# Kernel tuning notes

Measured on AMD Instinct MI355X. Metric: run time of the kernel, lower is better.

Reference implementation:

```python
import jax, jax.numpy as jnp
import numpy as np
import math

B, N, NODE_DIM, EDGE_DIM, HID, NH = 2, 384, 128, 128, 128, 8
HD = HID // NH  # head_dim = 16


def _layernorm(x, g, b, eps=1e-5):
    m = jnp.mean(x, axis=-1, keepdims=True)
    v = jnp.var(x, axis=-1, keepdims=True)
    return (x - m) * jax.lax.rsqrt(v + eps) * g + b


def setup_inputs() -> dict:
    key = jax.random.key(0)
    ks = jax.random.split(key, 16)
    w = lambda k, s: jax.random.normal(k, s, jnp.float32) * 0.05
    return {
        "node_features": jax.random.normal(ks[0], (B, N, NODE_DIM), jnp.float32),
        "edge_features": jax.random.normal(ks[1], (B, N, N, EDGE_DIM), jnp.float32),
        "adj_mask": jax.random.randint(ks[2], (B, N, N), 0, 2, jnp.int32),
        "W_node": w(ks[3], (NODE_DIM, HID)), "b_node": jnp.zeros((HID,), jnp.float32),
        "W_q": w(ks[4], (HID, HID)), "b_q": jnp.zeros((HID,), jnp.float32),
        "W_k": w(ks[5], (HID, HID)), "b_k": jnp.zeros((HID,), jnp.float32),
        "W_v": w(ks[6], (HID, HID)), "b_v": jnp.zeros((HID,), jnp.float32),
        "W_edge": w(ks[7], (EDGE_DIM, HID)), "b_edge": jnp.zeros((HID,), jnp.float32),
        "W_gate": w(ks[8], (EDGE_DIM, HID)), "b_gate": jnp.zeros((HID,), jnp.float32),
        "W_out": w(ks[9], (HID, HID)), "b_out": jnp.zeros((HID,), jnp.float32),
        "W_eout": w(ks[10], (HID, EDGE_DIM)), "b_eout": jnp.zeros((EDGE_DIM,), jnp.float32),
        "g1": jnp.ones((HID,), jnp.float32), "be1": jnp.zeros((HID,), jnp.float32),
        "g2": jnp.ones((EDGE_DIM,), jnp.float32), "be2": jnp.zeros((EDGE_DIM,), jnp.float32),
    }


def reference(node_features, edge_features, adj_mask,
              W_node, b_node, W_q, b_q, W_k, b_k, W_v, b_v,
              W_edge, b_edge, W_gate, b_gate, W_out, b_out,
              W_eout, b_eout, g1, be1, g2, be2):
    b, n, _ = node_features.shape
    h = node_features @ W_node + b_node          # (B,N,HID)
    residual = h
    Q = (h @ W_q + b_q).reshape(b, n, NH, HD)
    K = (h @ W_k + b_k).reshape(b, n, NH, HD)
    V = (h @ W_v + b_v).reshape(b, n, NH, HD)
    scores = jnp.einsum('bihd,bjhd->bhij', Q, K) / math.sqrt(HD)  # (B,NH,N,N)
    # edge-gated bias
    edge_h = (edge_features @ W_edge + b_edge).reshape(b, n, n, NH, HD)
    edge_gate = jax.nn.sigmoid(edge_features @ W_gate + b_gate).reshape(b, n, n, NH, HD)
    edge_attn = jnp.sum(edge_h * edge_gate, axis=-1)  # (B,N,N,NH)
    scores = scores + jnp.transpose(edge_attn, (0, 3, 1, 2))
    # adjacency mask
    scores = jnp.where(adj_mask[:, None, :, :] == 0, jnp.float32(-1e9), scores)
    attn = jax.nn.softmax(scores, axis=-1)  # dropout = identity (eval)
    attn_out = jnp.einsum('bhij,bjhd->bihd', attn, V).reshape(b, n, HID)
    h = _layernorm(residual + (attn_out @ W_out + b_out), g1, be1)
    # edge update: mean attention over heads gates (src+tgt)/2
    attn_mean = jnp.mean(attn, axis=1)  # (B,N,N)
    pair = 0.5 * (h[:, :, None, :] + h[:, None, :, :])  # (B,N,N,HID)
    edge_update = attn_mean[..., None] * pair
    edge_out = _layernorm(edge_features + (edge_update @ W_eout + b_eout), g2, be2)
    return h, edge_out
```

## Files before the change

### kernel.cpp

```cpp
#include <hip/hip_runtime.h>
#include <hip/hip_bf16.h>

#define NN 384
#define HIDDIM 128
#define NHEADS 8
#define HD 16
#define LOCAL_E (NN*NN)
#define NE (2*LOCAL_E)
#define NNODE (2*NN)

typedef __attribute__((ext_vector_type(8))) __bf16 bf16x8;
typedef __attribute__((ext_vector_type(4))) float f32x4;

__global__ void prep_w(const float* __restrict__ W_edge, const float* __restrict__ W_gate,
                       bf16x8* __restrict__ Wg) {
    int gid = blockIdx.x * blockDim.x + threadIdx.x;
    int n16  = gid & 15;
    int quad = (gid >> 4) & 3;
    int kkl  = (gid >> 6) & 1;
    int np   = (gid >> 7) & 15;
    int kkh  = (gid >> 11) & 1;
    int n = np * 16 + n16;
    int k0 = (kkh * 2 + kkl) * 32 + quad * 8;
    const float* src = (n < 128) ? (W_edge + n) : (W_gate + (n - 128));
    bf16x8 v;
#pragma unroll
    for (int j = 0; j < 8; ++j) v[j] = (__bf16)src[(size_t)(k0 + j) * 128];
    Wg[gid] = v;
}

__global__ __launch_bounds__(128) void k1_proj(
    const float* __restrict__ nf,
    const float* __restrict__ Wn, const float* __restrict__ bn,
    const float* __restrict__ Wq, const float* __restrict__ bq,
    const float* __restrict__ Wk, const float* __restrict__ bk,
    const float* __restrict__ Wv, const float* __restrict__ bv,
    float* __restrict__ h_res, float* __restrict__ Q,
    float* __restrict__ K, float* __restrict__ V)
{
    __shared__ float xf[8][128];
    __shared__ float hf[8][128];
    int t = threadIdx.x;
    int r0 = blockIdx.x * 8;
    for (int r = 0; r < 8; ++r) xf[r][t] = nf[(size_t)(r0 + r) * 128 + t];
    __syncthreads();
    float acc[8];
#pragma unroll
    for (int r = 0; r < 8; ++r) acc[r] = bn[t];
    for (int k = 0; k < 128; ++k) {
        float w = Wn[k * 128 + t];
#pragma unroll
        for (int r = 0; r < 8; ++r) acc[r] += xf[r][k] * w;
    }
    for (int r = 0; r < 8; ++r) { h_res[(size_t)(r0 + r) * 128 + t] = acc[r]; hf[r][t] = acc[r]; }
    __syncthreads();
    const float* Ws[3] = {Wq, Wk, Wv};
    const float* bs[3] = {bq, bk, bv};
    float* Os[3] = {Q, K, V};
#pragma unroll
    for (int m = 0; m < 3; ++m) {
        float a2[8];
#pragma unroll
        for (int r = 0; r < 8; ++r) a2[r] = bs[m][t];
        for (int k = 0; k < 128; ++k) {
            float w = Ws[m][k * 128 + t];
#pragma unroll
            for (int r = 0; r < 8; ++r) a2[r] += hf[r][k] * w;
        }
        int hh = t >> 4, d = t & 15;
        for (int r = 0; r < 8; ++r) {
            int g = r0 + r;
            int b = g / NN, i = g - b * NN;
            Os[m][(size_t)((b * NHEADS + hh) * NN + i) * HD + d] = a2[r];
        }
    }
}

__global__ __launch_bounds__(512, 4) void k2_edge(
    const float* __restrict__ EF, const bf16x8* __restrict__ Wg,
    const float* __restrict__ b_edge, const float* __restrict__ b_gate,
    float* __restrict__ edge_attn)
{
    __shared__ bf16x8 Ash[1024];
    __shared__ bf16x8 Bsh[2048];
    int t = threadIdx.x;
    int lane = t & 63;
    int w = t >> 6;
    int wm = w & 1, wn = w >> 1;
    int e_base = blockIdx.x * 128;

    f32x4 acc[4][4];
    f32x4 zero = {0.f, 0.f, 0.f, 0.f};
#pragma unroll
    for (int i = 0; i < 4; ++i)
#pragma unroll
        for (int j = 0; j < 4; ++j) acc[i][j] = zero;

    for (int kkh = 0; kkh < 2; ++kkh) {
#pragma unroll
        for (int p = 0; p < 4; ++p) {
            int g = p * 512 + t;
            Bsh[g] = Wg[kkh * 2048 + g];
        }
#pragma unroll
        for (int p = 0; p < 2; ++p) {
            int gid = p * 512 + t;
            int m16 = gid & 15, quad = (gid >> 4) & 3, kkl = (gid >> 6) & 1, ip = gid >> 7;
            int row = ip * 16 + m16;
            const float4* src4 = (const float4*)(EF + (size_t)(e_base + row) * 128
                                                 + (kkh * 2 + kkl) * 32 + quad * 8);
            float4 f0 = src4[0], f1 = src4[1];
            bf16x8 v;
            v[0] = (__bf16)f0.x; v[1] = (__bf16)f0.y; v[2] = (__bf16)f0.z; v[3] = (__bf16)f0.w;
            v[4] = (__bf16)f1.x; v[5] = (__bf16)f1.y; v[6] = (__bf16)f1.z; v[7] = (__bf16)f1.w;
            Ash[gid] = v;
        }
        __syncthreads();
#pragma unroll
        for (int kkl = 0; kkl < 2; ++kkl) {
            bf16x8 af[4], bfh[2], bfg[2];
#pragma unroll
            for (int i = 0; i < 4; ++i) {
                int ip = wm * 4 + i;
                af[i] = Ash[(ip * 2 + kkl) * 64 + lane];
            }
#pragma unroll
            for (int j = 0; j < 2; ++j) {
                int nph = wn * 2 + j;
                bfh[j] = Bsh[(nph * 2 + kkl) * 64 + lane];
                bfg[j] = Bsh[((nph + 8) * 2 + kkl) * 64 + lane];
            }
#pragma unroll
            for (int i = 0; i < 4; ++i) {
#pragma unroll
                for (int j = 0; j < 2; ++j) {
                    acc[i][j]     = __builtin_amdgcn_mfma_f32_16x16x32_bf16(af[i], bfh[j], acc[i][j], 0, 0, 0);
                    acc[i][j + 2] = __builtin_amdgcn_mfma_f32_16x16x32_bf16(af[i], bfg[j], acc[i][j + 2], 0, 0, 0);
                }
            }
        }
        __syncthreads();
    }

    int n16 = lane & 15, quad = lane >> 4;
#pragma unroll
    for (int j = 0; j < 2; ++j) {
        int c = wn * 32 + j * 16 + n16;
        float bh = b_edge[c], bg = b_gate[c];
        int head = wn * 2 + j;
#pragma unroll
        for (int i = 0; i < 4; ++i) {
#pragma unroll
            for (int r = 0; r < 4; ++r) {
                float hv = acc[i][j][r] + bh;
                float gv = acc[i][j + 2][r] + bg;
                float v = hv * (1.f / (1.f + __expf(-gv)));
                v += __shfl_xor(v, 1);
                v += __shfl_xor(v, 2);
                v += __shfl_xor(v, 4);
                v += __shfl_xor(v, 8);
                if (n16 == 0) {
                    int m = wm * 64 + i * 16 + quad * 4 + r;
                    int e = e_base + m;
                    int b = e / LOCAL_E;
                    int local = e - b * LOCAL_E;
                    edge_attn[(size_t)(b * NHEADS + head) * LOCAL_E + local] = v;
                }
            }
        }
    }
}

__global__ __launch_bounds__(128) void k3_attn(
    const float* __restrict__ Q, const float* __restrict__ K, const float* __restrict__ V,
    const float* __restrict__ edge_attn, const int* __restrict__ adj,
    float* __restrict__ am, float* __restrict__ attn_out)
{
    __shared__ float Kh[NN * 17];
    __shared__ float Vh[NN * 17];
    __shared__ float Qi[16 * HD];
    __shared__ float rowbuf[NN];
    __shared__ float red[2];
    __shared__ float red2[8][16];
    int t = threadIdx.x;
    int bh = blockIdx.x / 24;
    int chunk = blockIdx.x % 24;
    int b = bh >> 3;
    const float* Kbase = K + (size_t)bh * NN * HD;
    const float* Vbase = V + (size_t)bh * NN * HD;
    for (int p = 0; p < 48; ++p) {
        int idx = p * 128 + t;
        int jj = idx >> 4, dd = idx & 15;
        Kh[jj * 17 + dd] = Kbase[idx];
        Vh[jj * 17 + dd] = Vbase[idx];
    }
    Qi[t]       = Q[(size_t)bh * NN * HD + chunk * 16 * HD + t];
    Qi[t + 128] = Q[(size_t)bh * NN * HD + chunk * 16 * HD + t + 128];
    __syncthreads();
    int lane = t & 63, wid = t >> 6;
    const float* ea = edge_attn + (size_t)bh * LOCAL_E;
    const int* adjb = adj + (size_t)b * LOCAL_E;
    for (int rr = 0; rr < 16; ++rr) {
        int i = chunk * 16 + rr;
        float s[3];
#pragma unroll
        for (int jj = 0; jj < 3; ++jj) {
            int j = t + jj * 128;
            float a = 0.f;
#pragma unroll
            for (int d = 0; d < 16; ++d) a += Qi[rr * 16 + d] * Kh[j * 17 + d];
            a = a * 0.25f + ea[(size_t)i * NN + j];
            if (adjb[(size_t)i * NN + j] == 0) a = -1e9f;
            s[jj] = a;
        }
        float mx = fmaxf(s[0], fmaxf(s[1], s[2]));
#pragma unroll
        for (int o = 1; o < 64; o <<= 1) mx = fmaxf(mx, __shfl_xor(mx, o));
        if (lane == 0) red[wid] = mx;
        __syncthreads();
        mx = fmaxf(red[0], red[1]);
        __syncthreads();
        float e0 = __expf(s[0] - mx), e1 = __expf(s[1] - mx), e2 = __expf(s[2] - mx);
        float sm = e0 + e1 + e2;
#pragma unroll
        for (int o = 1; o < 64; o <<= 1) sm += __shfl_xor(sm, o);
        if (lane == 0) red[wid] = sm;
        __syncthreads();
        float inv = 1.f / (red[0] + red[1]);
        float p0 = e0 * inv, p1 = e1 * inv, p2 = e2 * inv;
        rowbuf[t] = p0; rowbuf[t + 128] = p1; rowbuf[t + 256] = p2;
        atomicAdd(am + (size_t)b * LOCAL_E + i * NN + t,       p0 * 0.125f);
        atomicAdd(am + (size_t)b * LOCAL_E + i * NN + t + 128, p1 * 0.125f);
        atomicAdd(am + (size_t)b * LOCAL_E + i * NN + t + 256, p2 * 0.125f);
        __syncthreads();
        int d = t & 15, g = t >> 4;
        float pa = 0.f;
        for (int j = g * 48; j < g * 48 + 48; ++j) pa += rowbuf[j] * Vh[j * 17 + d];
        red2[g][d] = pa;
        __syncthreads();
        if (t < 16) {
            float s2 = 0.f;
#pragma unroll
            for (int gg = 0; gg < 8; ++gg) s2 += red2[gg][t];
            attn_out[(size_t)(b * NN + i) * HIDDIM + (bh & 7) * HD + t] = s2;
        }
        __syncthreads();
    }
}

__global__ __launch_bounds__(128) void k5_hout(
    const float* __restrict__ attn_out, const float* __restrict__ h_res,
    const float* __restrict__ W_out, const float* __restrict__ b_out,
    const float* __restrict__ g1, const float* __restrict__ be1,
    const float* __restrict__ W_eout,
    float* __restrict__ h_out, float* __restrict__ hp)
{
    __shared__ float ao[8][128];
    __shared__ float hn[8][128];
    __shared__ float redA[2], redB[2];
    int t = threadIdx.x, r0 = blockIdx.x * 8;
    for (int r = 0; r < 8; ++r) ao[r][t] = attn_out[(size_t)(r0 + r) * 128 + t];
    __syncthreads();
    float acc[8];
#pragma unroll
    for (int r = 0; r < 8; ++r) acc[r] = b_out[t];
    for (int k = 0; k < 128; ++k) {
        float w = W_out[k * 128 + t];
#pragma unroll
        for (int r = 0; r < 8; ++r) acc[r] += ao[r][k] * w;
    }
    int lane = t & 63, wid = t >> 6;
    float gg = g1[t], bb = be1[t];
    for (int r = 0; r < 8; ++r) {
        float u = h_res[(size_t)(r0 + r) * 128 + t] + acc[r];
        float sv = u, sq = u * u;
#pragma unroll
        for (int o = 1; o < 64; o <<= 1) { sv += __shfl_xor(sv, o); sq += __shfl_xor(sq, o); }
        if (lane == 0) { redA[wid] = sv; redB[wid] = sq; }
        __syncthreads();
        float tot = redA[0] + redA[1], totq = redB[0] + redB[1];
        __syncthreads();
        float mean = tot * (1.f / 128.f);
        float var = totq * (1.f / 128.f) - mean * mean;
        float nv = (u - mean) * rsqrtf(var + 1e-5f) * gg + bb;
        h_out[(size_t)(r0 + r) * 128 + t] = nv;
        hn[r][t] = nv;
    }
    __syncthreads();
    float acc2[8];
#pragma unroll
    for (int r = 0; r < 8; ++r) acc2[r] = 0.f;
    for (int k = 0; k < 128; ++k) {
        float w = W_eout[k * 128 + t];
#pragma unroll
        for (int r = 0; r < 8; ++r) acc2[r] += hn[r][k] * w;
    }
    for (int r = 0; r < 8; ++r) hp[(size_t)(r0 + r) * 128 + t] = acc2[r];
}

__global__ __launch_bounds__(256) void k6_eout(
    const float* __restrict__ EF, const float* __restrict__ am,
    const float* __restrict__ hp, const float* __restrict__ b_eout,
    const float* __restrict__ g2, const float* __restrict__ be2,
    float* __restrict__ eout)
{
    int t = threadIdx.x;
    int slot = t >> 5, l = t & 31;
    int e = blockIdx.x * 8 + slot;
    int b = e / LOCAL_E;
    int local = e - b * LOCAL_E;
    int i = local / NN, j = local - i * NN;
    float a = am[e];
    const float4* ef4 = (const float4*)(EF + (size_t)e * 128);
    const float4* hpi = (const float4*)(hp + (size_t)(b * NN + i) * 128);
    const float4* hpj = (const float4*)(hp + (size_t)(b * NN + j) * 128);
    float4 ef = ef4[l];
    float4 pi = hpi[l], pj = hpj[l];
    float4 bo = ((const float4*)b_eout)[l];
    float4 u;
    u.x = ef.x + a * 0.5f * (pi.x + pj.x) + bo.x;
    u.y = ef.y + a * 0.5f * (pi.y + pj.y) + bo.y;
    u.z = ef.z + a * 0.5f * (pi.z + pj.z) + bo.z;
    u.w = ef.w + a * 0.5f * (pi.w + pj.w) + bo.w;
    float sv = u.x + u.y + u.z + u.w;
    float sq = u.x * u.x + u.y * u.y + u.z * u.z + u.w * u.w;
#pragma unroll
    for (int o = 1; o < 32; o <<= 1) { sv += __shfl_xor(sv, o); sq += __shfl_xor(sq, o); }
    float mean = sv * (1.f / 128.f);
    float var = sq * (1.f / 128.f) - mean * mean;
    float rs = rsqrtf(var + 1e-5f);
    float4 gg = ((const float4*)g2)[l], bb = ((const float4*)be2)[l];
    float4 o4;
    o4.x = (u.x - mean) * rs * gg.x + bb.x;
    o4.y = (u.y - mean) * rs * gg.y + bb.y;
    o4.z = (u.z - mean) * rs * gg.z + bb.z;
    o4.w = (u.w - mean) * rs * gg.w + bb.w;
    ((float4*)(eout + (size_t)e * 128))[l] = o4;
}

extern "C" void kernel_launch(void* const* d_in, const int* in_sizes, int n_in,
                              void* d_out, int out_size, void* d_ws, size_t ws_size,
                              hipStream_t stream) {
    (void)in_sizes; (void)n_in; (void)out_size; (void)ws_size;
    const float* nf     = (const float*)d_in[0];
    const float* ef     = (const float*)d_in[1];
    const int*   adj    = (const int*)d_in[2];
    const float* W_node = (const float*)d_in[3];
    const float* b_node = (const float*)d_in[4];
    const float* W_q    = (const float*)d_in[5];
    const float* b_q    = (const float*)d_in[6];
    const float* W_k    = (const float*)d_in[7];
    const float* b_k    = (const float*)d_in[8];
    const float* W_v    = (const float*)d_in[9];
    const float* b_v    = (const float*)d_in[10];
    const float* W_edge = (const float*)d_in[11];
    const float* b_edge = (const float*)d_in[12];
    const float* W_gate = (const float*)d_in[13];
    const float* b_gate = (const float*)d_in[14];
    const float* W_out  = (const float*)d_in[15];
    const float* b_out  = (const float*)d_in[16];
    const float* W_eout = (const float*)d_in[17];
    const float* b_eout = (const float*)d_in[18];
    const float* g1     = (const float*)d_in[19];
    const float* be1    = (const float*)d_in[20];
    const float* g2     = (const float*)d_in[21];
    const float* be2    = (const float*)d_in[22];

    float* ws = (float*)d_ws;
    float* h_res    = ws;
    float* Q        = ws + 98304;
    float* Kp       = ws + 196608;
    float* Vp       = ws + 294912;
    float* attn_out = ws + 393216;
    float* hp       = ws + 491520;
    float* am       = ws + 589824;
    bf16x8* Wg      = (bf16x8*)(ws + 884736);

    float* h_out = (float*)d_out;
    float* eout  = (float*)d_out + 98304;
    float* edge_attn = eout;

    prep_w<<<dim3(16), dim3(256), 0, stream>>>(W_edge, W_gate, Wg);
    k1_proj<<<dim3(96), dim3(128), 0, stream>>>(nf, W_node, b_node, W_q, b_q,
                                                W_k, b_k, W_v, b_v, h_res, Q, Kp, Vp);
    k2_edge<<<dim3(2304), dim3(512), 0, stream>>>(ef, Wg, b_edge, b_gate, edge_attn);
    hipMemsetAsync((void*)am, 0, (size_t)NE * sizeof(float), stream);
    k3_attn<<<dim3(384), dim3(128), 0, stream>>>(Q, Kp, Vp, edge_attn, adj, am, attn_out);
    k5_hout<<<dim3(96), dim3(128), 0, stream>>>(attn_out, h_res, W_out, b_out,
                                                g1, be1, W_eout, h_out, hp);
    k6_eout<<<dim3(36864), dim3(256), 0, stream>>>(ef, am, hp, b_eout, g2, be2, eout);
}
```

Before: 483.1 us.

## Persistent wave-tiled edge GEMM, fold mask into edge bias, drop atomics

The edge projection kernel becomes a persistent kernel. Each wave loops over 16-edge tiles, keeps all 256 weight columns resident in LDS and prefetches the next tile's edge features into registers. The adjacency mask is applied there, so the attention kernel no longer reads adj. The attention kernel is restructured to one row per wave with K/V stored transposed, with no block-level syncs, and it writes per-head attention probabilities. The atomic head-mean and its memset are removed: k6 now sums the 8 heads itself, at the cost of extra workspace and extra attention-map traffic.

```diff
diff --git a/kernel.cpp b/kernel.cpp
--- a/kernel.cpp
+++ b/kernel.cpp
@@ -7,7 +7,8 @@
 #define HD 16
 #define LOCAL_E (NN*NN)
 #define NE (2*LOCAL_E)
-#define NNODE (2*NN)
+#define NTILES (NE/16)
+#define NWAVES_K2 4096
 
 typedef __attribute__((ext_vector_type(8))) __bf16 bf16x8;
 typedef __attribute__((ext_vector_type(4))) float f32x4;
@@ -17,12 +18,11 @@
     int gid = blockIdx.x * blockDim.x + threadIdx.x;
     int n16  = gid & 15;
     int quad = (gid >> 4) & 3;
-    int kkl  = (gid >> 6) & 1;
-    int np   = (gid >> 7) & 15;
-    int kkh  = (gid >> 11) & 1;
-    int n = np * 16 + n16;
-    int k0 = (kkh * 2 + kkl) * 32 + quad * 8;
-    const float* src = (n < 128) ? (W_edge + n) : (W_gate + (n - 128));
+    int kk   = (gid >> 6) & 3;
+    int cg   = gid >> 8;
+    int col = cg * 16 + n16;
+    int k0 = kk * 32 + quad * 8;
+    const float* src = (col < 128) ? (W_edge + col) : (W_gate + (col - 128));
     bf16x8 v;
 #pragma unroll
     for (int j = 0; j < 8; ++j) v[j] = (__bf16)src[(size_t)(k0 + j) * 128];
@@ -76,175 +76,188 @@
     }
 }
 
-__global__ __launch_bounds__(512, 4) void k2_edge(
+__global__ __launch_bounds__(512, 2) void k2_edge(
     const float* __restrict__ EF, const bf16x8* __restrict__ Wg,
     const float* __restrict__ b_edge, const float* __restrict__ b_gate,
-    float* __restrict__ edge_attn)
+    const int* __restrict__ adj, float* __restrict__ ea)
 {
-    __shared__ bf16x8 Ash[1024];
-    __shared__ bf16x8 Bsh[2048];
+    __shared__ bf16x8 Bsh[4096];
     int t = threadIdx.x;
     int lane = t & 63;
     int w = t >> 6;
-    int wm = w & 1, wn = w >> 1;
-    int e_base = blockIdx.x * 128;
-
-    f32x4 acc[4][4];
-    f32x4 zero = {0.f, 0.f, 0.f, 0.f};
-#pragma unroll
-    for (int i = 0; i < 4; ++i)
-#pragma unroll
-        for (int j = 0; j < 4; ++j) acc[i][j] = zero;
-
-    for (int kkh = 0; kkh < 2; ++kkh) {
-#pragma unroll
-        for (int p = 0; p < 4; ++p) {
-            int g = p * 512 + t;
-            Bsh[g] = Wg[kkh * 2048 + g];
-        }
-#pragma unroll
-        for (int p = 0; p < 2; ++p) {
-            int gid = p * 512 + t;
-            int m16 = gid & 15, quad = (gid >> 4) & 3, kkl = (gid >> 6) & 1, ip = gid >> 7;
-            int row = ip * 16 + m16;
-            const float4* src4 = (const float4*)(EF + (size_t)(e_base + row) * 128
-                                                 + (kkh * 2 + kkl) * 32 + quad * 8);
-            float4 f0 = src4[0], f1 = src4[1];
+#pragma unroll
+    for (int p = 0; p < 8; ++p) {
+        int g = p * 512 + t;
+        Bsh[g] = Wg[g];
+    }
+    __syncthreads();
+
+    int n16 = lane & 15, quad = lane >> 4;
+    float bhv[8], bgv[8];
+#pragma unroll
+    for (int h = 0; h < 8; ++h) {
+        bhv[h] = b_edge[h * 16 + n16];
+        bgv[h] = b_gate[h * 16 + n16];
+    }
+
+    int gw = blockIdx.x * 8 + w;
+    int tile = gw;
+
+    float4 f[8];
+    const float* ar0 = EF + ((size_t)tile * 16 + n16) * 128 + quad * 8;
+#pragma unroll
+    for (int kk = 0; kk < 4; ++kk) {
+        f[2 * kk]     = *(const float4*)(ar0 + kk * 32);
+        f[2 * kk + 1] = *(const float4*)(ar0 + kk * 32 + 4);
+    }
+
+    while (tile < NTILES) {
+        int next = tile + NWAVES_K2;
+        bf16x8 af[4];
+#pragma unroll
+        for (int kk = 0; kk < 4; ++kk) {
+            float4 f0 = f[2 * kk], f1 = f[2 * kk + 1];
             bf16x8 v;
             v[0] = (__bf16)f0.x; v[1] = (__bf16)f0.y; v[2] = (__bf16)f0.z; v[3] = (__bf16)f0.w;
             v[4] = (__bf16)f1.x; v[5] = (__bf16)f1.y; v[6] = (__bf16)f1.z; v[7] = (__bf16)f1.w;
-            Ash[gid] = v;
-        }
-        __syncthreads();
-#pragma unroll
-        for (int kkl = 0; kkl < 2; ++kkl) {
-            bf16x8 af[4], bfh[2], bfg[2];
-#pragma unroll
-            for (int i = 0; i < 4; ++i) {
-                int ip = wm * 4 + i;
-                af[i] = Ash[(ip * 2 + kkl) * 64 + lane];
+            af[kk] = v;
+        }
+        if (next < NTILES) {
+            const float* ar = EF + ((size_t)next * 16 + n16) * 128 + quad * 8;
+#pragma unroll
+            for (int kk = 0; kk < 4; ++kk) {
+                f[2 * kk]     = *(const float4*)(ar + kk * 32);
+                f[2 * kk + 1] = *(const float4*)(ar + kk * 32 + 4);
             }
-#pragma unroll
-            for (int j = 0; j < 2; ++j) {
-                int nph = wn * 2 + j;
-                bfh[j] = Bsh[(nph * 2 + kkl) * 64 + lane];
-                bfg[j] = Bsh[((nph + 8) * 2 + kkl) * 64 + lane];
+        }
+
+        f32x4 acc[8][2];
+        f32x4 zero = {0.f, 0.f, 0.f, 0.f};
+#pragma unroll
+        for (int h = 0; h < 8; ++h) { acc[h][0] = zero; acc[h][1] = zero; }
+#pragma unroll
+        for (int kk = 0; kk < 4; ++kk) {
+#pragma unroll
+            for (int h = 0; h < 8; ++h) {
+                bf16x8 bh = Bsh[(h * 4 + kk) * 64 + lane];
+                bf16x8 bg = Bsh[((8 + h) * 4 + kk) * 64 + lane];
+                acc[h][0] = __builtin_amdgcn_mfma_f32_16x16x32_bf16(af[kk], bh, acc[h][0], 0, 0, 0);
+                acc[h][1] = __builtin_amdgcn_mfma_f32_16x16x32_bf16(af[kk], bg, acc[h][1], 0, 0, 0);
             }
-#pragma unroll
-            for (int i = 0; i < 4; ++i) {
-#pragma unroll
-                for (int j = 0; j < 2; ++j) {
-                    acc[i][j]     = __builtin_amdgcn_mfma_f32_16x16x32_bf16(af[i], bfh[j], acc[i][j], 0, 0, 0);
-                    acc[i][j + 2] = __builtin_amdgcn_mfma_f32_16x16x32_bf16(af[i], bfg[j], acc[i][j + 2], 0, 0, 0);
-                }
-            }
-        }
-        __syncthreads();
-    }
-
-    int n16 = lane & 15, quad = lane >> 4;
-#pragma unroll
-    for (int j = 0; j < 2; ++j) {
-        int c = wn * 32 + j * 16 + n16;
-        float bh = b_edge[c], bg = b_gate[c];
-        int head = wn * 2 + j;
-#pragma unroll
-        for (int i = 0; i < 4; ++i) {
+        }
+
+        size_t e0 = (size_t)tile * 16;
+        int b = (tile >= NTILES / 2) ? 1 : 0;
+        int local0 = (int)(e0 - (size_t)b * LOCAL_E);
+        const int* adjp = adj + (size_t)b * LOCAL_E + local0 + quad * 4;
+        int av0 = adjp[0], av1 = adjp[1], av2 = adjp[2], av3 = adjp[3];
+#pragma unroll
+        for (int h = 0; h < 8; ++h) {
+            float vr[4];
 #pragma unroll
             for (int r = 0; r < 4; ++r) {
-                float hv = acc[i][j][r] + bh;
-                float gv = acc[i][j + 2][r] + bg;
+                float hv = acc[h][0][r] + bhv[h];
+                float gv = acc[h][1][r] + bgv[h];
                 float v = hv * (1.f / (1.f + __expf(-gv)));
                 v += __shfl_xor(v, 1);
                 v += __shfl_xor(v, 2);
                 v += __shfl_xor(v, 4);
                 v += __shfl_xor(v, 8);
-                if (n16 == 0) {
-                    int m = wm * 64 + i * 16 + quad * 4 + r;
-                    int e = e_base + m;
-                    int b = e / LOCAL_E;
-                    int local = e - b * LOCAL_E;
-                    edge_attn[(size_t)(b * NHEADS + head) * LOCAL_E + local] = v;
-                }
+                vr[r] = v;
             }
-        }
-    }
-}
-
-__global__ __launch_bounds__(128) void k3_attn(
+            if (n16 == 0) {
+                float4 o;
+                o.x = av0 ? vr[0] : -1e9f;
+                o.y = av1 ? vr[1] : -1e9f;
+                o.z = av2 ? vr[2] : -1e9f;
+                o.w = av3 ? vr[3] : -1e9f;
+                *(float4*)(ea + ((size_t)(b * 8 + h)) * LOCAL_E + local0 + quad * 4) = o;
+            }
+        }
+        tile = next;
+    }
+}
+
+__global__ __launch_bounds__(256) void k3_attn(
     const float* __restrict__ Q, const float* __restrict__ K, const float* __restrict__ V,
-    const float* __restrict__ edge_attn, const int* __restrict__ adj,
-    float* __restrict__ am, float* __restrict__ attn_out)
+    const float* __restrict__ ea, float* __restrict__ attn,
+    float* __restrict__ attn_out)
 {
-    __shared__ float Kh[NN * 17];
-    __shared__ float Vh[NN * 17];
-    __shared__ float Qi[16 * HD];
-    __shared__ float rowbuf[NN];
-    __shared__ float red[2];
-    __shared__ float red2[8][16];
+    __shared__ float Kt[16 * 385];
+    __shared__ float Vt[16 * 385];
+    __shared__ float Qi[256];
+    __shared__ float prow[4][384];
     int t = threadIdx.x;
     int bh = blockIdx.x / 24;
     int chunk = blockIdx.x % 24;
-    int b = bh >> 3;
+    int b = bh >> 3, h = bh & 7;
     const float* Kbase = K + (size_t)bh * NN * HD;
     const float* Vbase = V + (size_t)bh * NN * HD;
-    for (int p = 0; p < 48; ++p) {
-        int idx = p * 128 + t;
-        int jj = idx >> 4, dd = idx & 15;
-        Kh[jj * 17 + dd] = Kbase[idx];
-        Vh[jj * 17 + dd] = Vbase[idx];
-    }
-    Qi[t]       = Q[(size_t)bh * NN * HD + chunk * 16 * HD + t];
-    Qi[t + 128] = Q[(size_t)bh * NN * HD + chunk * 16 * HD + t + 128];
-    __syncthreads();
-    int lane = t & 63, wid = t >> 6;
-    const float* ea = edge_attn + (size_t)bh * LOCAL_E;
-    const int* adjb = adj + (size_t)b * LOCAL_E;
-    for (int rr = 0; rr < 16; ++rr) {
-        int i = chunk * 16 + rr;
-        float s[3];
-#pragma unroll
-        for (int jj = 0; jj < 3; ++jj) {
-            int j = t + jj * 128;
+    for (int p = 0; p < 24; ++p) {
+        int idx = p * 256 + t;
+        int j = idx >> 4, d = idx & 15;
+        Kt[d * 385 + j] = Kbase[idx];
+        Vt[d * 385 + j] = Vbase[idx];
+    }
+    Qi[t] = Q[(size_t)bh * NN * HD + chunk * 256 + t];
+    __syncthreads();
+
+    int lane = t & 63, w = t >> 6;
+    for (int ri = 0; ri < 4; ++ri) {
+        int r_local = w * 4 + ri;
+        int i = chunk * 16 + r_local;
+        float4 q0 = *(const float4*)&Qi[r_local * 16 + 0];
+        float4 q1 = *(const float4*)&Qi[r_local * 16 + 4];
+        float4 q2 = *(const float4*)&Qi[r_local * 16 + 8];
+        float4 q3 = *(const float4*)&Qi[r_local * 16 + 12];
+        const float* eaI = ea + (size_t)bh * LOCAL_E + (size_t)i * NN;
+        float s[6];
+#pragma unroll
+        for (int jj = 0; jj < 6; ++jj) {
+            int j = jj * 64 + lane;
             float a = 0.f;
-#pragma unroll
-            for (int d = 0; d < 16; ++d) a += Qi[rr * 16 + d] * Kh[j * 17 + d];
-            a = a * 0.25f + ea[(size_t)i * NN + j];
-            if (adjb[(size_t)i * NN + j] == 0) a = -1e9f;
-            s[jj] = a;
-        }
-        float mx = fmaxf(s[0], fmaxf(s[1], s[2]));
+            a += q0.x * Kt[0 * 385 + j];  a += q0.y * Kt[1 * 385 + j];
+            a += q0.z * Kt[2 * 385 + j];  a += q0.w * Kt[3 * 385 + j];
+            a += q1.x * Kt[4 * 385 + j];  a += q1.y * Kt[5 * 385 + j];
+            a += q1.z * Kt[6 * 385 + j];  a += q1.w * Kt[7 * 385 + j];
+            a += q2.x * Kt[8 * 385 + j];  a += q2.y * Kt[9 * 385 + j];
+            a += q2.z * Kt[10 * 385 + j]; a += q2.w * Kt[11 * 385 + j];
+            a += q3.x * Kt[12 * 385 + j]; a += q3.y * Kt[13 * 385 + j];
+            a += q3.z * Kt[14 * 385 + j]; a += q3.w * Kt[15 * 385 + j];
+            s[jj] = a * 0.25f + eaI[j];
+        }
+        float mx = s[0];
+#pragma unroll
+        for (int jj = 1; jj < 6; ++jj) mx = fmaxf(mx, s[jj]);
 #pragma unroll
         for (int o = 1; o < 64; o <<= 1) mx = fmaxf(mx, __shfl_xor(mx, o));
-        if (lane == 0) red[wid] = mx;
-        __syncthreads();
-        mx = fmaxf(red[0], red[1]);
-        __syncthreads();
-        float e0 = __expf(s[0] - mx), e1 = __expf(s[1] - mx), e2 = __expf(s[2] - mx);
-        float sm = e0 + e1 + e2;
+        float sm = 0.f;
+        float e[6];
+#pragma unroll
+        for (int jj = 0; jj < 6; ++jj) { e[jj] = __expf(s[jj] - mx); sm += e[jj]; }
 #pragma unroll
         for (int o = 1; o < 64; o <<= 1) sm += __shfl_xor(sm, o);
-        if (lane == 0) red[wid] = sm;
-        __syncthreads();
-        float inv = 1.f / (red[0] + red[1]);
-        float p0 = e0 * inv, p1 = e1 * inv, p2 = e2 * inv;
-        rowbuf[t] = p0; rowbuf[t + 128] = p1; rowbuf[t + 256] = p2;
-        atomicAdd(am + (size_t)b * LOCAL_E + i * NN + t,       p0 * 0.125f);
-        atomicAdd(am + (size_t)b * LOCAL_E + i * NN + t + 128, p1 * 0.125f);
-        atomicAdd(am + (size_t)b * LOCAL_E + i * NN + t + 256, p2 * 0.125f);
-        __syncthreads();
-        int d = t & 15, g = t >> 4;
-        float pa = 0.f;
-        for (int j = g * 48; j < g * 48 + 48; ++j) pa += rowbuf[j] * Vh[j * 17 + d];
-        red2[g][d] = pa;
-        __syncthreads();
-        if (t < 16) {
-            float s2 = 0.f;
-#pragma unroll
-            for (int gg = 0; gg < 8; ++gg) s2 += red2[gg][t];
-            attn_out[(size_t)(b * NN + i) * HIDDIM + (bh & 7) * HD + t] = s2;
-        }
-        __syncthreads();
+        float inv = 1.f / sm;
+        float* attnI = attn + (size_t)bh * LOCAL_E + (size_t)i * NN;
+#pragma unroll
+        for (int jj = 0; jj < 6; ++jj) {
+            float p = e[jj] * inv;
+            attnI[jj * 64 + lane] = p;
+            prow[w][jj * 64 + lane] = p;
+        }
+        int d = lane & 15, g = lane >> 4;
+        float o = 0.f;
+#pragma unroll
+        for (int jt = 0; jt < 24; ++jt) {
+            int j = g * 96 + jt * 4;
+            float4 pp = *(const float4*)&prow[w][j];
+            o += pp.x * Vt[d * 385 + j]     + pp.y * Vt[d * 385 + j + 1]
+               + pp.z * Vt[d * 385 + j + 2] + pp.w * Vt[d * 385 + j + 3];
+        }
+        o += __shfl_xor(o, 16);
+        o += __shfl_xor(o, 32);
+        if (lane < 16)
+            attn_out[((size_t)b * NN + i) * HIDDIM + h * HD + d] = o;
     }
 }
 
@@ -299,19 +312,24 @@
 }
 
 __global__ __launch_bounds__(256) void k6_eout(
-    const float* __restrict__ EF, const float* __restrict__ am,
+    const float* __restrict__ EF, const float* __restrict__ attn,
     const float* __restrict__ hp, const float* __restrict__ b_eout,
     const float* __restrict__ g2, const float* __restrict__ be2,
     float* __restrict__ eout)
 {
     int t = threadIdx.x;
     int slot = t >> 5, l = t & 31;
-    int e = blockIdx.x * 8 + slot;
-    int b = e / LOCAL_E;
-    int local = e - b * LOCAL_E;
+    size_t e = (size_t)blockIdx.x * 8 + slot;
+    int b = (int)(e / LOCAL_E);
+    int local = (int)(e - (size_t)b * LOCAL_E);
     int i = local / NN, j = local - i * NN;
-    float a = am[e];
-    const float4* ef4 = (const float4*)(EF + (size_t)e * 128);
+    float av = 0.f;
+    if (l < 8) av = attn[((size_t)(b * 8 + l)) * LOCAL_E + local];
+    av += __shfl_xor(av, 1, 32);
+    av += __shfl_xor(av, 2, 32);
+    av += __shfl_xor(av, 4, 32);
+    float a = __shfl(av, 0, 32) * 0.125f;
+    const float4* ef4 = (const float4*)(EF + e * 128);
     const float4* hpi = (const float4*)(hp + (size_t)(b * NN + i) * 128);
     const float4* hpj = (const float4*)(hp + (size_t)(b * NN + j) * 128);
     float4 ef = ef4[l];
@@ -325,7 +343,7 @@
     float sv = u.x + u.y + u.z + u.w;
     float sq = u.x * u.x + u.y * u.y + u.z * u.z + u.w * u.w;
 #pragma unroll
-    for (int o = 1; o < 32; o <<= 1) { sv += __shfl_xor(sv, o); sq += __shfl_xor(sq, o); }
+    for (int o = 1; o < 32; o <<= 1) { sv += __shfl_xor(sv, o, 32); sq += __shfl_xor(sq, o, 32); }
     float mean = sv * (1.f / 128.f);
     float var = sq * (1.f / 128.f) - mean * mean;
     float rs = rsqrtf(var + 1e-5f);
@@ -335,7 +353,7 @@
     o4.y = (u.y - mean) * rs * gg.y + bb.y;
     o4.z = (u.z - mean) * rs * gg.z + bb.z;
     o4.w = (u.w - mean) * rs * gg.w + bb.w;
-    ((float4*)(eout + (size_t)e * 128))[l] = o4;
+    ((float4*)(eout + e * 128))[l] = o4;
 }
 
 extern "C" void kernel_launch(void* const* d_in, const int* in_sizes, int n_in,
@@ -373,20 +391,19 @@
     float* Vp       = ws + 294912;
     float* attn_out = ws + 393216;
     float* hp       = ws + 491520;
-    float* am       = ws + 589824;
-    bf16x8* Wg      = (bf16x8*)(ws + 884736);
+    bf16x8* Wg      = (bf16x8*)(ws + 589824);
+    float* attn     = ws + 606208;
 
     float* h_out = (float*)d_out;
     float* eout  = (float*)d_out + 98304;
-    float* edge_attn = eout;
+    float* ea = eout;
 
     prep_w<<<dim3(16), dim3(256), 0, stream>>>(W_edge, W_gate, Wg);
     k1_proj<<<dim3(96), dim3(128), 0, stream>>>(nf, W_node, b_node, W_q, b_q,
                                                 W_k, b_k, W_v, b_v, h_res, Q, Kp, Vp);
-    k2_edge<<<dim3(2304), dim3(512), 0, stream>>>(ef, Wg, b_edge, b_gate, edge_attn);
-    hipMemsetAsync((void*)am, 0, (size_t)NE * sizeof(float), stream);
-    k3_attn<<<dim3(384), dim3(128), 0, stream>>>(Q, Kp, Vp, edge_attn, adj, am, attn_out);
+    k2_edge<<<dim3(512), dim3(512), 0, stream>>>(ef, Wg, b_edge, b_gate, adj, ea);
+    k3_attn<<<dim3(384), dim3(256), 0, stream>>>(Q, Kp, Vp, ea, attn, attn_out);
     k5_hout<<<dim3(96), dim3(128), 0, stream>>>(attn_out, h_res, W_out, b_out,
                                                 g1, be1, W_eout, h_out, hp);
-    k6_eout<<<dim3(36864), dim3(256), 0, stream>>>(ef, am, hp, b_eout, g2, be2, eout);
-}
+    k6_eout<<<dim3(36864), dim3(256), 0, stream>>>(ef, attn, hp, b_eout, g2, be2, eout);
+}
```

New measurement: 599.5 us. 24.1% more time.
